# Performance work log

Hardware: AMD Instinct MI355X
Metric: run time of the kernel (lower is better)

The kernel has to match this reference:

```python
import jax, jax.numpy as jnp
import numpy as np

N, E = 20000, 320000
IN_C, HID, OUT_C, HEADS = 512, 32, 40, 8
NEG_SLOPE = 0.2


def setup_inputs() -> dict:
    key = jax.random.key(0)
    ks = jax.random.split(key, 10)
    x = jax.random.normal(ks[0], (N, IN_C), dtype=jnp.float32)
    edge_index = jax.random.randint(ks[1], (2, E), 0, N, dtype=jnp.int64)
    s1 = 1.0 / np.sqrt(IN_C)
    s2 = 1.0 / np.sqrt(HEADS * HID)
    return {
        "x": x,
        "edge_index": edge_index,
        "w1": jax.random.normal(ks[2], (IN_C, HEADS * HID), dtype=jnp.float32) * s1,
        "att_src1": jax.random.normal(ks[3], (HEADS, HID), dtype=jnp.float32) * s2,
        "att_dst1": jax.random.normal(ks[4], (HEADS, HID), dtype=jnp.float32) * s2,
        "b1": jnp.zeros((HEADS * HID,), dtype=jnp.float32),
        "w2": jax.random.normal(ks[5], (HEADS * HID, OUT_C), dtype=jnp.float32) * s2,
        "att_src2": jax.random.normal(ks[6], (1, OUT_C), dtype=jnp.float32) * 0.15,
        "att_dst2": jax.random.normal(ks[7], (1, OUT_C), dtype=jnp.float32) * 0.15,
        "b2": jnp.zeros((OUT_C,), dtype=jnp.float32),
    }


def gat_conv(x, src, dst, w, att_src, att_dst, bias, heads, out_c, concat):
    n = x.shape[0]
    h = (x @ w).reshape(n, heads, out_c)            # [N,H,C]
    a_s = jnp.sum(h * att_src, axis=-1)             # [N,H]
    a_d = jnp.sum(h * att_dst, axis=-1)             # [N,H]
    e = jax.nn.leaky_relu(a_s[src] + a_d[dst], NEG_SLOPE)  # [E,H]
    # segment softmax over destination nodes (self-loops guarantee nonempty)
    m = jax.ops.segment_max(e, dst, num_segments=n)
    e = jnp.exp(e - m[dst])
    z = jax.ops.segment_sum(e, dst, num_segments=n)
    alpha = e / (z[dst] + 1e-16)                    # [E,H]
    msg = alpha[:, :, None] * h[src]                # [E,H,C]
    out = jax.ops.segment_sum(msg, dst, num_segments=n)  # [N,H,C]
    out = out.reshape(n, heads * out_c) if concat else out.mean(axis=1)
    return out + bias


def reference(x, edge_index, w1, att_src1, att_dst1, b1, w2, att_src2, att_dst2, b2):
    n = x.shape[0]
    loops = jnp.arange(n, dtype=edge_index.dtype)
    src = jnp.concatenate([edge_index[0], loops])
    dst = jnp.concatenate([edge_index[1], loops])
    h = gat_conv(x, src, dst, w1, att_src1, att_dst1, b1, HEADS, HID, True)
    h = jax.nn.elu(h)
    out = gat_conv(h, src, dst, w2, att_src2, att_dst2, b2, 1, OUT_C, False)
    return jax.nn.log_softmax(out, axis=1)
```

## Files before the change

kernel.cpp:

```cpp
#include <hip/hip_runtime.h>
#include <hip/hip_bf16.h>
#include <math.h>

#define N_NODES 20000
#define N_EDGES 320000
#define ET (N_EDGES + N_NODES)
#define IN_C 512
#define HEADS 8
#define HID 32
#define HH (HEADS * HID)
#define OUT_C 40
#define NEG_SLOPE 0.2f

typedef __attribute__((ext_vector_type(8))) short short8;
typedef __attribute__((ext_vector_type(4))) float floatx4;

static __device__ __forceinline__ unsigned short f2bf(float f) {
  __hip_bfloat16 h = __float2bfloat16(f);
  return *(unsigned short*)&h;
}
static __device__ __forceinline__ float bf2f_lo(unsigned int u) {
  return __uint_as_float(u << 16);
}
static __device__ __forceinline__ float bf2f_hi(unsigned int u) {
  return __uint_as_float(u & 0xFFFF0000u);
}

#define WCONV_BLOCKS (IN_C * HH / 256)
#define W2CONV_BLOCKS (HH * OUT_C / 256)
#define COUNT_BLOCKS ((ET + 255) / 256)
__global__ __launch_bounds__(256) void prep_kernel(
    const float* __restrict__ w1, const float* __restrict__ w2,
    const int* __restrict__ ei, unsigned short* __restrict__ wbT,
    unsigned short* __restrict__ w2bT, int* __restrict__ deg) {
  if (blockIdx.x < WCONV_BLOCKS) {
    int j = blockIdx.x * 256 + threadIdx.x;
    int k = j >> 8, n = j & 255;
    wbT[(size_t)n * IN_C + k] = f2bf(w1[j]);
  } else if (blockIdx.x < WCONV_BLOCKS + W2CONV_BLOCKS) {
    int j = (blockIdx.x - WCONV_BLOCKS) * 256 + threadIdx.x;
    int k = j / OUT_C, oc = j % OUT_C;
    w2bT[oc * HH + k] = f2bf(w2[j]);
  } else {
    int e = (blockIdx.x - WCONV_BLOCKS - W2CONV_BLOCKS) * 256 + threadIdx.x;
    if (e < ET) {
      int dst = (e < N_EDGES) ? ei[N_EDGES + e] : (e - N_EDGES);
      atomicAdd(&deg[dst], 1);
    }
  }
}

#define BM 64
#define BN 128
#define BK 32
#define APAD 40
#define GY ((N_NODES + BM - 1) / BM)
#define GEMM_BLOCKS (2 * GY)
__global__ __launch_bounds__(256) void gemm1_kernel(
    const float* __restrict__ X, const unsigned short* __restrict__ BT,
    const float* __restrict__ bias, unsigned short* __restrict__ C,
    const int* __restrict__ deg, int* __restrict__ offs, int* __restrict__ cursor) {
  if (blockIdx.x >= GEMM_BLOCKS) {
    __shared__ int wsum[4];
    int t = threadIdx.x;
    int4 buf[20];
    int s = 0;
    if (t < 250) {
      const int4* dp = (const int4*)deg + t * 20;
#pragma unroll
      for (int i = 0; i < 20; i++) {
        buf[i] = dp[i];
        s += buf[i].x + buf[i].y + buf[i].z + buf[i].w;
      }
    }
    int lane = t & 63, w = t >> 6;
    int inc = s;
    for (int o = 1; o < 64; o <<= 1) {
      int u = __shfl_up(inc, o, 64);
      if (lane >= o) inc += u;
    }
    if (lane == 63) wsum[w] = inc;
    __syncthreads();
    int waveOff = 0;
    for (int i = 0; i < w; i++) waveOff += wsum[i];
    int running = waveOff + inc - s;
    if (t < 250) {
      int base = t * 80;
#pragma unroll
      for (int i = 0; i < 20; i++) {
        int4 v = buf[i];
        int4 o;
        o.x = running;
        o.y = o.x + v.x;
        o.z = o.y + v.y;
        o.w = o.z + v.z;
        running = o.w + v.w;
        *(int4*)(offs + base + i * 4) = o;
        *(int4*)(cursor + base + i * 4) = o;
      }
    }
    if (t == 0) offs[N_NODES] = ET;
    return;
  }
  __shared__ unsigned short As[BM][APAD];
  __shared__ unsigned short Bs[BN][APAD];
  const int tid = threadIdx.x;
  const int lane = tid & 63, wave = tid >> 6;
  const int wm = (wave & 1) * 32;
  const int wn = (wave >> 1) * 64;
  const int r16 = lane & 15, q = lane >> 4;
  const int bx = blockIdx.x & 1, by = blockIdx.x >> 1;
  const int rowBase = by * BM;
  const int colBase = bx * BN;
  floatx4 acc[2][4] = {};

  for (int k0 = 0; k0 < IN_C; k0 += BK) {
    {
      int row = tid >> 2, kc = (tid & 3) * 8;
      int arow = rowBase + row;
      float4 v0 = make_float4(0.f, 0.f, 0.f, 0.f), v1 = v0;
      if (arow < N_NODES) {
        const float* p = X + (size_t)arow * IN_C + k0 + kc;
        v0 = *(const float4*)p;
        v1 = *(const float4*)(p + 4);
      }
      unsigned short tmp[8] = {f2bf(v0.x), f2bf(v0.y), f2bf(v0.z), f2bf(v0.w),
                               f2bf(v1.x), f2bf(v1.y), f2bf(v1.z), f2bf(v1.w)};
      *(float4*)&As[row][kc] = *(const float4*)tmp;
    }
#pragma unroll
    for (int i = 0; i < 2; i++) {
      int c = tid + i * 256;
      int row = c >> 2, kc = (c & 3) * 8;
      float4 v = *(const float4*)(BT + (size_t)(colBase + row) * IN_C + k0 + kc);
      *(float4*)&Bs[row][kc] = v;
    }
    __syncthreads();
    short8 afrag[2], bfrag[4];
#pragma unroll
    for (int mt = 0; mt < 2; mt++)
      afrag[mt] = *(const short8*)&As[wm + mt * 16 + r16][q * 8];
#pragma unroll
    for (int nt = 0; nt < 4; nt++)
      bfrag[nt] = *(const short8*)&Bs[wn + nt * 16 + r16][q * 8];
#pragma unroll
    for (int mt = 0; mt < 2; mt++)
#pragma unroll
      for (int nt = 0; nt < 4; nt++)
        acc[mt][nt] = __builtin_amdgcn_mfma_f32_16x16x32_bf16(
            afrag[mt], bfrag[nt], acc[mt][nt], 0, 0, 0);
    __syncthreads();
  }
#pragma unroll
  for (int mt = 0; mt < 2; mt++) {
#pragma unroll
    for (int nt = 0; nt < 4; nt++) {
      int col = colBase + wn + nt * 16 + r16;
      float bb = bias[col];
#pragma unroll
      for (int r = 0; r < 4; r++) {
        int row = rowBase + wm + mt * 16 + q * 4 + r;
        if (row < N_NODES) C[(size_t)row * HH + col] = f2bf(acc[mt][nt][r] + bb);
      }
    }
  }
}

#define FILL_BLOCKS ((ET + 255) / 256)
#define ATTN1_BLOCKS (N_NODES / 4)
__global__ __launch_bounds__(256) void fill_attn1_kernel(
    const int* __restrict__ ei, int* __restrict__ cursor, int* __restrict__ csr,
    const unsigned short* __restrict__ h1b, const float* __restrict__ asrc,
    const float* __restrict__ adst, float* __restrict__ as1, float* __restrict__ ad1) {
  if (blockIdx.x < FILL_BLOCKS) {
    int e = blockIdx.x * 256 + threadIdx.x;
    if (e >= ET) return;
    int src, dst;
    if (e < N_EDGES) { src = ei[e]; dst = ei[N_EDGES + e]; }
    else { src = e - N_EDGES; dst = src; }
    int pos = atomicAdd(&cursor[dst], 1);
    csr[pos] = src;
  } else {
    int wave = threadIdx.x >> 6, lane = threadIdx.x & 63;
    int n = (blockIdx.x - FILL_BLOCKS) * 4 + wave;
    int c4 = lane * 4;
    uint2 raw = *(const uint2*)(h1b + (size_t)n * HH + c4);
    float h0 = bf2f_lo(raw.x), h1 = bf2f_hi(raw.x);
    float h2 = bf2f_lo(raw.y), h3 = bf2f_hi(raw.y);
    float4 sa = *(const float4*)(asrc + c4);
    float4 sd = *(const float4*)(adst + c4);
    float ps = h0 * sa.x + h1 * sa.y + h2 * sa.z + h3 * sa.w;
    float pd = h0 * sd.x + h1 * sd.y + h2 * sd.z + h3 * sd.w;
#pragma unroll
    for (int o = 4; o > 0; o >>= 1) {
      ps += __shfl_down(ps, o, 8);
      pd += __shfl_down(pd, o, 8);
    }
    if ((lane & 7) == 0) {
      as1[n * HEADS + (lane >> 3)] = ps;
      ad1[n * HEADS + (lane >> 3)] = pd;
    }
  }
}

#define NPB 16
#define H2ROW 264
__global__ __launch_bounds__(256) void layer1_fused_kernel(
    const unsigned short* __restrict__ h1b, const float* __restrict__ as1,
    const float* __restrict__ ad1, const int* __restrict__ offs,
    const int* __restrict__ csr, const float* __restrict__ b1,
    const unsigned short* __restrict__ w2bT, const float* __restrict__ b2,
    const float* __restrict__ asrc2, const float* __restrict__ adst2,
    float* __restrict__ h3, float* __restrict__ as2, float* __restrict__ ad2) {
  __shared__ __align__(16) unsigned short h2s[NPB][H2ROW];
  __shared__ float psum[3][NPB], pdsum[3][NPB];
  const int tid = threadIdx.x;
  const int wave = tid >> 6, lane = tid & 63;
  const int r16 = lane & 15, q = lane >> 4;
  const int nodeBase = blockIdx.x * NPB;

  short8 bfrag[8];
  float sa = 0.f, sd = 0.f, b2c = 0.f;
  if (wave < 3) {
    int col = wave * 16 + r16;
    int colc = (col < OUT_C) ? col : 0;
#pragma unroll
    for (int s = 0; s < 8; s++)
      bfrag[s] = *(const short8*)(w2bT + colc * HH + s * 32 + q * 8);
    if (col < OUT_C) { sa = asrc2[col]; sd = adst2[col]; b2c = b2[col]; }
  }

  const int strm = lane >> 4;
  const int l16 = lane & 15;
  const int c16 = l16 * 16;
  const int head = l16 >> 1;
  float4 bb0 = *(const float4*)(b1 + c16);
  float4 bb1 = *(const float4*)(b1 + c16 + 4);
  float4 bb2 = *(const float4*)(b1 + c16 + 8);
  float4 bb3 = *(const float4*)(b1 + c16 + 12);
  for (int i = 0; i < 4; i++) {
    int local = wave * 4 + i;
    int n = nodeBase + local;
    int beg = offs[n], end = offs[n + 1];
    float ad = ad1[n * HEADS + head];
    float acc[16] = {};
    float l = 0.f;
#pragma unroll 2
    for (int k = beg + strm; k < end; k += 4) {
      int src = csr[k];
      float e = as1[src * HEADS + head] + ad;
      e = (e > 0.f) ? e : NEG_SLOPE * e;
      float p = __expf(e);
      l += p;
      const unsigned short* hp = h1b + ((unsigned)src << 8) + c16;
      uint4 r0 = *(const uint4*)hp;
      uint4 r1 = *(const uint4*)(hp + 8);
      acc[0]  = fmaf(p, bf2f_lo(r0.x), acc[0]);
      acc[1]  = fmaf(p, bf2f_hi(r0.x), acc[1]);
      acc[2]  = fmaf(p, bf2f_lo(r0.y), acc[2]);
      acc[3]  = fmaf(p, bf2f_hi(r0.y), acc[3]);
      acc[4]  = fmaf(p, bf2f_lo(r0.z), acc[4]);
      acc[5]  = fmaf(p, bf2f_hi(r0.z), acc[5]);
      acc[6]  = fmaf(p, bf2f_lo(r0.w), acc[6]);
      acc[7]  = fmaf(p, bf2f_hi(r0.w), acc[7]);
      acc[8]  = fmaf(p, bf2f_lo(r1.x), acc[8]);
      acc[9]  = fmaf(p, bf2f_hi(r1.x), acc[9]);
      acc[10] = fmaf(p, bf2f_lo(r1.y), acc[10]);
      acc[11] = fmaf(p, bf2f_hi(r1.y), acc[11]);
      acc[12] = fmaf(p, bf2f_lo(r1.z), acc[12]);
      acc[13] = fmaf(p, bf2f_hi(r1.z), acc[13]);
      acc[14] = fmaf(p, bf2f_lo(r1.w), acc[14]);
      acc[15] = fmaf(p, bf2f_hi(r1.w), acc[15]);
    }
#pragma unroll
    for (int j = 0; j < 16; j++) {
      acc[j] += __shfl_xor(acc[j], 16, 64);
      acc[j] += __shfl_xor(acc[j], 32, 64);
    }
    l += __shfl_xor(l, 16, 64);
    l += __shfl_xor(l, 32, 64);
    if (strm == 0) {
      float li = 1.f / (l + 1e-16f);
      float v[16];
      v[0]  = acc[0]  * li + bb0.x; v[1]  = acc[1]  * li + bb0.y;
      v[2]  = acc[2]  * li + bb0.z; v[3]  = acc[3]  * li + bb0.w;
      v[4]  = acc[4]  * li + bb1.x; v[5]  = acc[5]  * li + bb1.y;
      v[6]  = acc[6]  * li + bb1.z; v[7]  = acc[7]  * li + bb1.w;
      v[8]  = acc[8]  * li + bb2.x; v[9]  = acc[9]  * li + bb2.y;
      v[10] = acc[10] * li + bb2.z; v[11] = acc[11] * li + bb2.w;
      v[12] = acc[12] * li + bb3.x; v[13] = acc[13] * li + bb3.y;
      v[14] = acc[14] * li + bb3.z; v[15] = acc[15] * li + bb3.w;
      unsigned short o16[16];
#pragma unroll
      for (int j = 0; j < 16; j++) {
        float e = (v[j] > 0.f) ? v[j] : expm1f(v[j]);
        o16[j] = f2bf(e);
      }
      *(uint4*)&h2s[local][c16] = *(const uint4*)&o16[0];
      *(uint4*)&h2s[local][c16 + 8] = *(const uint4*)&o16[8];
    }
  }
  __syncthreads();

  if (wave < 3) {
    floatx4 dacc = {};
#pragma unroll
    for (int s = 0; s < 8; s++) {
      short8 afrag = *(const short8*)&h2s[r16][s * 32 + q * 8];
      dacc = __builtin_amdgcn_mfma_f32_16x16x32_bf16(afrag, bfrag[s], dacc, 0, 0, 0);
    }
    int col = wave * 16 + r16;
    float psr[4], pdr[4];
#pragma unroll
    for (int r = 0; r < 4; r++) {
      float val = dacc[r] + b2c;
      if (col < OUT_C)
        h3[(size_t)(nodeBase + q * 4 + r) * OUT_C + col] = val;
      psr[r] = val * sa;
      pdr[r] = val * sd;
    }
#pragma unroll
    for (int o = 8; o > 0; o >>= 1) {
#pragma unroll
      for (int r = 0; r < 4; r++) {
        psr[r] += __shfl_down(psr[r], o, 16);
        pdr[r] += __shfl_down(pdr[r], o, 16);
      }
    }
    if (r16 == 0) {
#pragma unroll
      for (int r = 0; r < 4; r++) {
        psum[wave][q * 4 + r] = psr[r];
        pdsum[wave][q * 4 + r] = pdr[r];
      }
    }
  }
  __syncthreads();
  if (tid < NPB) {
    as2[nodeBase + tid] = psum[0][tid] + psum[1][tid] + psum[2][tid];
    ad2[nodeBase + tid] = pdsum[0][tid] + pdsum[1][tid] + pdsum[2][tid];
  }
}

__global__ __launch_bounds__(256) void agg2_kernel(
    const float* __restrict__ h3, const float* __restrict__ as2,
    const float* __restrict__ ad2, const int* __restrict__ offs,
    const int* __restrict__ csr, const float* __restrict__ b2,
    float* __restrict__ out) {
  int n = blockIdx.x * 4 + (threadIdx.x >> 6);
  int t = threadIdx.x & 63;
  bool act = (t < OUT_C);
  int beg = offs[n], end = offs[n + 1];
  float ad = ad2[n];
  float l0 = 0.f, l1 = 0.f, a0 = 0.f, a1 = 0.f;
  int k = beg;
  for (; k + 1 < end; k += 2) {
    int s0 = csr[k], s1 = csr[k + 1];
    float e0 = as2[s0] + ad, e1 = as2[s1] + ad;
    e0 = (e0 > 0.f) ? e0 : NEG_SLOPE * e0;
    e1 = (e1 > 0.f) ? e1 : NEG_SLOPE * e1;
    float p0 = __expf(e0), p1 = __expf(e1);
    l0 += p0; l1 += p1;
    float h0 = act ? h3[(size_t)s0 * OUT_C + t] : 0.f;
    float h1 = act ? h3[(size_t)s1 * OUT_C + t] : 0.f;
    a0 = fmaf(p0, h0, a0);
    a1 = fmaf(p1, h1, a1);
  }
  if (k < end) {
    int s0 = csr[k];
    float e0 = as2[s0] + ad;
    e0 = (e0 > 0.f) ? e0 : NEG_SLOPE * e0;
    float p0 = __expf(e0);
    l0 += p0;
    float h0 = act ? h3[(size_t)s0 * OUT_C + t] : 0.f;
    a0 = fmaf(p0, h0, a0);
  }
  float l = l0 + l1, acc = a0 + a1;
  float v = acc / (l + 1e-16f) + (act ? b2[t] : 0.f);
  float x = act ? v : -INFINITY;
  float mx = x;
  for (int o = 32; o > 0; o >>= 1) mx = fmaxf(mx, __shfl_down(mx, o, 64));
  mx = __shfl(mx, 0, 64);
  float ex = act ? __expf(v - mx) : 0.f;
  float s = ex;
  for (int o = 32; o > 0; o >>= 1) s += __shfl_down(s, o, 64);
  s = __shfl(s, 0, 64);
  if (act) out[(size_t)n * OUT_C + t] = v - mx - logf(s);
}

extern "C" void kernel_launch(void* const* d_in, const int* in_sizes, int n_in,
                              void* d_out, int out_size, void* d_ws, size_t ws_size,
                              hipStream_t stream) {
  const float* x     = (const float*)d_in[0];
  const int*   ei    = (const int*)d_in[1];
  const float* w1    = (const float*)d_in[2];
  const float* asrc1 = (const float*)d_in[3];
  const float* adst1 = (const float*)d_in[4];
  const float* b1    = (const float*)d_in[5];
  const float* w2    = (const float*)d_in[6];
  const float* asrc2 = (const float*)d_in[7];
  const float* adst2 = (const float*)d_in[8];
  const float* b2    = (const float*)d_in[9];
  float* out = (float*)d_out;

  float* fw = (float*)d_ws;
  float* as1   = fw;  fw += (size_t)N_NODES * HEADS;
  float* ad1   = fw;  fw += (size_t)N_NODES * HEADS;
  float* h3    = fw;  fw += (size_t)N_NODES * OUT_C;
  float* as2   = fw;  fw += N_NODES;
  float* ad2   = fw;  fw += N_NODES;
  unsigned short* h1b  = (unsigned short*)fw;  fw += (size_t)N_NODES * HH / 2;
  unsigned short* wbT  = (unsigned short*)fw;  fw += (size_t)IN_C * HH / 2;
  unsigned short* w2bT = (unsigned short*)fw;  fw += (size_t)HH * OUT_C / 2;
  int* deg    = (int*)fw;
  int* offs   = deg + N_NODES;
  int* cursor = offs + N_NODES + 4;
  int* csr    = cursor + N_NODES;

  hipMemsetAsync(deg, 0, N_NODES * sizeof(int), stream);

  prep_kernel<<<WCONV_BLOCKS + W2CONV_BLOCKS + COUNT_BLOCKS, 256, 0, stream>>>(
      w1, w2, ei, wbT, w2bT, deg);
  gemm1_kernel<<<GEMM_BLOCKS + 1, 256, 0, stream>>>(x, wbT, b1, h1b, deg, offs, cursor);
  fill_attn1_kernel<<<FILL_BLOCKS + ATTN1_BLOCKS, 256, 0, stream>>>(
      ei, cursor, csr, h1b, asrc1, adst1, as1, ad1);
  layer1_fused_kernel<<<N_NODES / NPB, 256, 0, stream>>>(
      h1b, as1, ad1, offs, csr, b1, w2bT, b2, asrc2, adst2, h3, as2, ad2);
  agg2_kernel<<<N_NODES / 4, 256, 0, stream>>>(h3, as2, ad2, offs, csr, b2, out);
}
```

Measured before the change: 234.2 us.

## Restructure layer-1 aggregation to 32 lanes per node with software-pipelined gathers

Changes the per-node gather from 4 streams of 16 lanes (16 channels each) to 2 streams of 32 lanes (8 channels each), halving accumulator registers and the cross-stream shuffle reduction. The edge loop is software-pipelined so the next neighbor's row and attention score load while the current one accumulates. ELU now uses __expf-1 instead of expm1f, spread across all lanes. The W2 fragment loads move after the barrier to lower register pressure. Fewer streams per node may reduce memory-level parallelism for high-degree nodes, and __expf-1 is slightly less accurate near zero.

New measurement: 220.3 us. 5.9% less time.

```diff
diff --git a/kernel.cpp b/kernel.cpp
--- a/kernel.cpp
+++ b/kernel.cpp
@@ -219,97 +219,88 @@
   const int r16 = lane & 15, q = lane >> 4;
   const int nodeBase = blockIdx.x * NPB;
 
-  short8 bfrag[8];
-  float sa = 0.f, sd = 0.f, b2c = 0.f;
-  if (wave < 3) {
-    int col = wave * 16 + r16;
-    int colc = (col < OUT_C) ? col : 0;
-#pragma unroll
-    for (int s = 0; s < 8; s++)
-      bfrag[s] = *(const short8*)(w2bT + colc * HH + s * 32 + q * 8);
-    if (col < OUT_C) { sa = asrc2[col]; sd = adst2[col]; b2c = b2[col]; }
-  }
-
-  const int strm = lane >> 4;
-  const int l16 = lane & 15;
-  const int c16 = l16 * 16;
-  const int head = l16 >> 1;
-  float4 bb0 = *(const float4*)(b1 + c16);
-  float4 bb1 = *(const float4*)(b1 + c16 + 4);
-  float4 bb2 = *(const float4*)(b1 + c16 + 8);
-  float4 bb3 = *(const float4*)(b1 + c16 + 12);
+  const int strm = lane >> 5;
+  const int l32 = lane & 31;
+  const int c8 = l32 * 8;
+  const int head = l32 >> 2;
+  float4 bb = *(const float4*)(b1 + c8 + strm * 4);
   for (int i = 0; i < 4; i++) {
     int local = wave * 4 + i;
     int n = nodeBase + local;
     int beg = offs[n], end = offs[n + 1];
     float ad = ad1[n * HEADS + head];
-    float acc[16] = {};
+    float acc[8] = {};
     float l = 0.f;
-#pragma unroll 2
-    for (int k = beg + strm; k < end; k += 4) {
+    int k = beg + strm;
+    if (k < end) {
       int src = csr[k];
-      float e = as1[src * HEADS + head] + ad;
-      e = (e > 0.f) ? e : NEG_SLOPE * e;
-      float p = __expf(e);
+      uint4 r = *(const uint4*)(h1b + ((unsigned)src << 8) + c8);
+      float e = as1[src * HEADS + head];
+      for (k += 2; k < end; k += 2) {
+        int src2 = csr[k];
+        uint4 r2 = *(const uint4*)(h1b + ((unsigned)src2 << 8) + c8);
+        float e2 = as1[src2 * HEADS + head];
+        float t = e + ad;
+        t = (t > 0.f) ? t : NEG_SLOPE * t;
+        float p = __expf(t);
+        l += p;
+        acc[0] = fmaf(p, bf2f_lo(r.x), acc[0]);
+        acc[1] = fmaf(p, bf2f_hi(r.x), acc[1]);
+        acc[2] = fmaf(p, bf2f_lo(r.y), acc[2]);
+        acc[3] = fmaf(p, bf2f_hi(r.y), acc[3]);
+        acc[4] = fmaf(p, bf2f_lo(r.z), acc[4]);
+        acc[5] = fmaf(p, bf2f_hi(r.z), acc[5]);
+        acc[6] = fmaf(p, bf2f_lo(r.w), acc[6]);
+        acc[7] = fmaf(p, bf2f_hi(r.w), acc[7]);
+        r = r2; e = e2;
+      }
+      float t = e + ad;
+      t = (t > 0.f) ? t : NEG_SLOPE * t;
+      float p = __expf(t);
       l += p;
-      const unsigned short* hp = h1b + ((unsigned)src << 8) + c16;
-      uint4 r0 = *(const uint4*)hp;
-      uint4 r1 = *(const uint4*)(hp + 8);
-      acc[0]  = fmaf(p, bf2f_lo(r0.x), acc[0]);
-      acc[1]  = fmaf(p, bf2f_hi(r0.x), acc[1]);
-      acc[2]  = fmaf(p, bf2f_lo(r0.y), acc[2]);
-      acc[3]  = fmaf(p, bf2f_hi(r0.y), acc[3]);
-      acc[4]  = fmaf(p, bf2f_lo(r0.z), acc[4]);
-      acc[5]  = fmaf(p, bf2f_hi(r0.z), acc[5]);
-      acc[6]  = fmaf(p, bf2f_lo(r0.w), acc[6]);
-      acc[7]  = fmaf(p, bf2f_hi(r0.w), acc[7]);
-      acc[8]  = fmaf(p, bf2f_lo(r1.x), acc[8]);
-      acc[9]  = fmaf(p, bf2f_hi(r1.x), acc[9]);
-      acc[10] = fmaf(p, bf2f_lo(r1.y), acc[10]);
-      acc[11] = fmaf(p, bf2f_hi(r1.y), acc[11]);
-      acc[12] = fmaf(p, bf2f_lo(r1.z), acc[12]);
-      acc[13] = fmaf(p, bf2f_hi(r1.z), acc[13]);
-      acc[14] = fmaf(p, bf2f_lo(r1.w), acc[14]);
-      acc[15] = fmaf(p, bf2f_hi(r1.w), acc[15]);
-    }
-#pragma unroll
-    for (int j = 0; j < 16; j++) {
-      acc[j] += __shfl_xor(acc[j], 16, 64);
-      acc[j] += __shfl_xor(acc[j], 32, 64);
-    }
-    l += __shfl_xor(l, 16, 64);
+      acc[0] = fmaf(p, bf2f_lo(r.x), acc[0]);
+      acc[1] = fmaf(p, bf2f_hi(r.x), acc[1]);
+      acc[2] = fmaf(p, bf2f_lo(r.y), acc[2]);
+      acc[3] = fmaf(p, bf2f_hi(r.y), acc[3]);
+      acc[4] = fmaf(p, bf2f_lo(r.z), acc[4]);
+      acc[5] = fmaf(p, bf2f_hi(r.z), acc[5]);
+      acc[6] = fmaf(p, bf2f_lo(r.w), acc[6]);
+      acc[7] = fmaf(p, bf2f_hi(r.w), acc[7]);
+    }
+#pragma unroll
+    for (int j = 0; j < 8; j++) acc[j] += __shfl_xor(acc[j], 32, 64);
     l += __shfl_xor(l, 32, 64);
-    if (strm == 0) {
-      float li = 1.f / (l + 1e-16f);
-      float v[16];
-      v[0]  = acc[0]  * li + bb0.x; v[1]  = acc[1]  * li + bb0.y;
-      v[2]  = acc[2]  * li + bb0.z; v[3]  = acc[3]  * li + bb0.w;
-      v[4]  = acc[4]  * li + bb1.x; v[5]  = acc[5]  * li + bb1.y;
-      v[6]  = acc[6]  * li + bb1.z; v[7]  = acc[7]  * li + bb1.w;
-      v[8]  = acc[8]  * li + bb2.x; v[9]  = acc[9]  * li + bb2.y;
-      v[10] = acc[10] * li + bb2.z; v[11] = acc[11] * li + bb2.w;
-      v[12] = acc[12] * li + bb3.x; v[13] = acc[13] * li + bb3.y;
-      v[14] = acc[14] * li + bb3.z; v[15] = acc[15] * li + bb3.w;
-      unsigned short o16[16];
-#pragma unroll
-      for (int j = 0; j < 16; j++) {
-        float e = (v[j] > 0.f) ? v[j] : expm1f(v[j]);
-        o16[j] = f2bf(e);
-      }
-      *(uint4*)&h2s[local][c16] = *(const uint4*)&o16[0];
-      *(uint4*)&h2s[local][c16 + 8] = *(const uint4*)&o16[8];
-    }
+    float li = 1.f / (l + 1e-16f);
+    float v0 = (strm ? acc[4] : acc[0]) * li + bb.x;
+    float v1 = (strm ? acc[5] : acc[1]) * li + bb.y;
+    float v2 = (strm ? acc[6] : acc[2]) * li + bb.z;
+    float v3 = (strm ? acc[7] : acc[3]) * li + bb.w;
+    v0 = (v0 > 0.f) ? v0 : __expf(v0) - 1.f;
+    v1 = (v1 > 0.f) ? v1 : __expf(v1) - 1.f;
+    v2 = (v2 > 0.f) ? v2 : __expf(v2) - 1.f;
+    v3 = (v3 > 0.f) ? v3 : __expf(v3) - 1.f;
+    uint2 w;
+    w.x = (unsigned)f2bf(v0) | ((unsigned)f2bf(v1) << 16);
+    w.y = (unsigned)f2bf(v2) | ((unsigned)f2bf(v3) << 16);
+    *(uint2*)&h2s[local][c8 + strm * 4] = w;
   }
   __syncthreads();
 
   if (wave < 3) {
+    int col = wave * 16 + r16;
+    int colc = (col < OUT_C) ? col : 0;
+    short8 bfrag[8];
+#pragma unroll
+    for (int s = 0; s < 8; s++)
+      bfrag[s] = *(const short8*)(w2bT + colc * HH + s * 32 + q * 8);
+    float sa = 0.f, sd = 0.f, b2c = 0.f;
+    if (col < OUT_C) { sa = asrc2[col]; sd = adst2[col]; b2c = b2[col]; }
     floatx4 dacc = {};
 #pragma unroll
     for (int s = 0; s < 8; s++) {
       short8 afrag = *(const short8*)&h2s[r16][s * 32 + q * 8];
       dacc = __builtin_amdgcn_mfma_f32_16x16x32_bf16(afrag, bfrag[s], dacc, 0, 0, 0);
     }
-    int col = wave * 16 + r16;
     float psr[4], pdr[4];
 #pragma unroll
     for (int r = 0; r < 4; r++) {
```
